# Performance work log

Hardware: AMD Instinct MI355X
Metric: run time of the kernel (lower is better)

The kernel has to match this reference:

```python
import jax, jax.numpy as jnp
import numpy as np

B, T, C = 4, 2048, 1024
H, DK, DV = 16, 64, 64  # num_heads, qk_length, value_length (must be equal per source bug)


def setup_inputs() -> dict:
    key = jax.random.key(0)
    ks = jax.random.split(key, 11)
    s = 0.02
    return {
        "Q": jax.random.normal(ks[0], (B, T, C), jnp.float32),
        "K": jax.random.normal(ks[1], (B, T, C), jnp.float32),
        "V": jax.random.normal(ks[2], (B, T, C), jnp.float32),
        "Wq": jax.random.normal(ks[3], (C, H * DK), jnp.float32) * s,
        "bq": jnp.zeros((H * DK,), jnp.float32),
        "Wk": jax.random.normal(ks[4], (C, H * DK), jnp.float32) * s,
        "bk": jnp.zeros((H * DK,), jnp.float32),
        "Wv": jax.random.normal(ks[5], (C, H * DK), jnp.float32) * s,
        "bv": jnp.zeros((H * DK,), jnp.float32),
        "Wo": jax.random.normal(ks[6], (H * DV, C), jnp.float32) * s,
        "bo": jnp.zeros((C,), jnp.float32),
    }


def _split_heads(x, d):
    # (B, T, H*d) -> (B, H, T, d)
    b, t, _ = x.shape
    return x.reshape(b, t, H, d).transpose(0, 2, 1, 3)


def reference(Q, K, V, Wq, bq, Wk, bk, Wv, bv, Wo, bo):
    q = _split_heads(Q @ Wq + bq, DK)  # (B,H,T,DK)
    k = _split_heads(K @ Wk + bk, DK)
    v = _split_heads(V @ Wv + bv, DV)
    scores = jnp.einsum("bhqd,bhkd->bhqk", q, k) / jnp.sqrt(jnp.float32(DK))
    weights = jax.nn.softmax(scores, axis=-1)  # materialized (B,H,T,T) as in source
    attn = jnp.einsum("bhqk,bhkd->bhqd", weights, v)  # (B,H,T,DV)
    # Faithful to source combine_heads: raw view (B,H,T,DV) -> (B,T,H*DV) WITHOUT transposing
    out = attn.reshape(B, T, H * DV)
    return out @ Wo + bo
```

## Files before the change

kernel.cpp:

```cpp
#include <hip/hip_runtime.h>

typedef unsigned short u16;
typedef __attribute__((ext_vector_type(8))) short bf16x8;
typedef __attribute__((ext_vector_type(4))) float f32x4;

__device__ __forceinline__ u16 f2bf(float f) {
  union { float fv; unsigned u; } v; v.fv = f;
  unsigned r = v.u + 0x7fffu + ((v.u >> 16) & 1u);
  return (u16)(r >> 16);
}

__device__ __forceinline__ unsigned pkbf(float a, float b) {
  union { float f; unsigned u; } ua, ub;
  ua.f = a; ub.f = b;
  return ((ub.u + 0x8000u) & 0xFFFF0000u) | ((ua.u + 0x8000u) >> 16);
}

__device__ __forceinline__ void gload_lds16(const void* g, void* l) {
  __builtin_amdgcn_global_load_lds(
      (const __attribute__((address_space(1))) unsigned*)g,
      (__attribute__((address_space(3))) unsigned*)l, 16, 0, 0);
}

__device__ __forceinline__ int swz128(int o) { return o ^ ((o >> 3) & 0x70); }
__device__ __forceinline__ int swz64(int o) { return o ^ (((o >> 7) & 3) << 4); }

__global__ __launch_bounds__(256) void transpose_cvt4_kernel(
    const float* __restrict__ W0, const float* __restrict__ W1,
    const float* __restrict__ W2, const float* __restrict__ W3,
    u16* __restrict__ T0, u16* __restrict__ T1,
    u16* __restrict__ T2, u16* __restrict__ T3) {
  __shared__ float tile[32][33];
  const int z = blockIdx.z;
  const float* W = z == 0 ? W0 : z == 1 ? W1 : z == 2 ? W2 : W3;
  u16* WT = z == 0 ? T0 : z == 1 ? T1 : z == 2 ? T2 : T3;
  const int bx = blockIdx.x * 32, by = blockIdx.y * 32;
  const int tx = threadIdx.x, ty = threadIdx.y;
  #pragma unroll
  for (int i = 0; i < 32; i += 8)
    tile[ty + i][tx] = W[(size_t)(by + ty + i) * 1024 + bx + tx];
  __syncthreads();
  #pragma unroll
  for (int i = 0; i < 32; i += 8)
    WT[(size_t)(bx + ty + i) * 1024 + by + tx] = f2bf(tile[tx][ty + i]);
}

__global__ __launch_bounds__(256) void proj_gemm_kernel(
    const float* __restrict__ Qf, const float* __restrict__ Kf,
    const float* __restrict__ Vf,
    const u16* __restrict__ WTq, const u16* __restrict__ WTk,
    const u16* __restrict__ WTv,
    const float* __restrict__ bqp, const float* __restrict__ bkp,
    const float* __restrict__ bvp,
    u16* __restrict__ qhd, u16* __restrict__ khd, u16* __restrict__ vtd) {
  __shared__ u16 As[128 * 32];
  __shared__ u16 Bs[128 * 32];
  const int tid = threadIdx.x;
  const int w = tid >> 6, lane = tid & 63;
  const int wr = w >> 1, wc = w & 1;
  const int l16 = lane & 15, lhi = lane >> 4;
  const int lg = (blockIdx.x & 7) * 192 + (blockIdx.x >> 3);
  const int proj = lg >> 9, inner = lg & 511;
  const int m0 = (inner >> 3) * 128, n0 = (inner & 7) * 128;
  const float* A  = proj == 0 ? Qf : proj == 1 ? Kf : Vf;
  const u16*   BT = proj == 0 ? WTq : proj == 1 ? WTk : WTv;
  const float* bias = proj == 0 ? bqp : proj == 1 ? bkp : bvp;

  const int arow = tid >> 2, ac = (tid & 3) * 8;

  f32x4 acc[4][4] = {};
  float4 pre[2][2];

  auto loadA = [&](int kt) {
    #pragma unroll
    for (int i = 0; i < 2; ++i) {
      const float* ap = A + (size_t)(m0 + arow + i * 64) * 1024 + kt * 32 + ac;
      pre[i][0] = *(const float4*)(ap);
      pre[i][1] = *(const float4*)(ap + 4);
    }
  };

  loadA(0);

  for (int kt = 0; kt < 32; ++kt) {
    #pragma unroll
    for (int i = 0; i < 2; ++i) {
      uint4 pk;
      pk.x = pkbf(pre[i][0].x, pre[i][0].y); pk.y = pkbf(pre[i][0].z, pre[i][0].w);
      pk.z = pkbf(pre[i][1].x, pre[i][1].y); pk.w = pkbf(pre[i][1].z, pre[i][1].w);
      const int lb = (arow + i * 64) * 64 + (tid & 3) * 16;
      *(uint4*)((char*)As + swz64(lb)) = pk;
    }
    #pragma unroll
    for (int i = 0; i < 2; ++i) {
      const int ob = w * 2048 + i * 1024;
      const int os = swz64(ob + (lane << 4));
      const int row = os >> 6, kb = os & 63;
      gload_lds16((const char*)BT + (((size_t)(n0 + row)) << 11) + (kt << 6) + kb,
                  (char*)Bs + ob);
    }
    __syncthreads();
    if (kt < 31) loadA(kt + 1);

    bf16x8 a[4], b[4];
    #pragma unroll
    for (int i = 0; i < 4; ++i)
      a[i] = *(const bf16x8*)((const char*)As +
             swz64((wr * 64 + i * 16 + l16) * 64 + lhi * 16));
    #pragma unroll
    for (int j = 0; j < 4; ++j)
      b[j] = *(const bf16x8*)((const char*)Bs +
             swz64((wc * 64 + j * 16 + l16) * 64 + lhi * 16));
    #pragma unroll
    for (int i = 0; i < 4; ++i)
      #pragma unroll
      for (int j = 0; j < 4; ++j)
        acc[i][j] = __builtin_amdgcn_mfma_f32_16x16x32_bf16(a[i], b[j], acc[i][j], 0, 0, 0);
    __syncthreads();
  }

  #pragma unroll
  for (int i = 0; i < 4; ++i) {
    #pragma unroll
    for (int j = 0; j < 4; ++j) {
      const int n = n0 + wc * 64 + j * 16 + l16;
      const float bn = bias[n];
      #pragma unroll
      for (int r = 0; r < 4; ++r) {
        const int m = m0 + wr * 64 + i * 16 + lhi * 4 + r;
        float v = acc[i][j][r] + bn;
        const int bb = m >> 11, t = m & 2047, h = n >> 6, d = n & 63;
        if (proj == 0) {
          v *= 0.18033688f;
          qhd[((((size_t)bb * 16 + h) * 2048 + t) << 6) + d] = f2bf(v);
        } else if (proj == 1) {
          khd[((((size_t)bb * 16 + h) * 2048 + t) << 6) + d] = f2bf(v);
        } else {
          vtd[(((size_t)bb * 16 + h) * 64 + d) * 2048 + t] = f2bf(v);
        }
      }
    }
  }
}

__global__ __launch_bounds__(256) void out_gemm_kernel(
    const u16* __restrict__ A, const u16* __restrict__ BT,
    const float* __restrict__ bias, float* __restrict__ out) {
  __shared__ u16 As[128 * 32];
  __shared__ u16 Bs[128 * 32];
  const int tid = threadIdx.x;
  const int w = tid >> 6, lane = tid & 63;
  const int wr = w >> 1, wc = w & 1;
  const int l16 = lane & 15, lhi = lane >> 4;
  const int lg = (blockIdx.x & 7) * 64 + (blockIdx.x >> 3);
  const int m0 = (lg >> 3) * 128, n0 = (lg & 7) * 128;

  f32x4 acc[4][4] = {};

  for (int kt = 0; kt < 32; ++kt) {
    #pragma unroll
    for (int i = 0; i < 2; ++i) {
      const int ob = w * 2048 + i * 1024;
      const int os = swz64(ob + (lane << 4));
      const int row = os >> 6, kb = os & 63;
      gload_lds16((const char*)A + (((size_t)(m0 + row)) << 11) + (kt << 6) + kb,
                  (char*)As + ob);
      gload_lds16((const char*)BT + (((size_t)(n0 + row)) << 11) + (kt << 6) + kb,
                  (char*)Bs + ob);
    }
    __syncthreads();
    bf16x8 a[4], b[4];
    #pragma unroll
    for (int i = 0; i < 4; ++i)
      a[i] = *(const bf16x8*)((const char*)As +
             swz64((wr * 64 + i * 16 + l16) * 64 + lhi * 16));
    #pragma unroll
    for (int j = 0; j < 4; ++j)
      b[j] = *(const bf16x8*)((const char*)Bs +
             swz64((wc * 64 + j * 16 + l16) * 64 + lhi * 16));
    #pragma unroll
    for (int i = 0; i < 4; ++i)
      #pragma unroll
      for (int j = 0; j < 4; ++j)
        acc[i][j] = __builtin_amdgcn_mfma_f32_16x16x32_bf16(a[i], b[j], acc[i][j], 0, 0, 0);
    __syncthreads();
  }

  #pragma unroll
  for (int i = 0; i < 4; ++i) {
    #pragma unroll
    for (int j = 0; j < 4; ++j) {
      const int n = n0 + wc * 64 + j * 16 + l16;
      const float bn = bias[n];
      #pragma unroll
      for (int r = 0; r < 4; ++r) {
        const int m = m0 + wr * 64 + i * 16 + lhi * 4 + r;
        out[(size_t)m * 1024 + n] = acc[i][j][r] + bn;
      }
    }
  }
}

__global__ __launch_bounds__(512) void attn_kernel(
    const u16* __restrict__ qh, const u16* __restrict__ kh,
    const u16* __restrict__ vth, u16* __restrict__ outPre) {
  __shared__ u16 Kbuf[2][64 * 64];
  __shared__ u16 Vbuf[64 * 64];
  __shared__ u16 Pl[8][16 * 64];

  const int tid = threadIdx.x, w = tid >> 6, lane = tid & 63;
  const int l16 = lane & 15, lhi = lane >> 4;

  const int wg = (blockIdx.x & 7) * 128 + (blockIdx.x >> 3);
  const int qt = wg & 15, hb = wg >> 4;
  const int h = hb & 15, b = hb >> 4;

  const size_t bh = (size_t)b * 16 + h;
  const u16* qb = qh + bh * (2048 * 64);
  const u16* kb = kh + bh * (2048 * 64);
  const u16* vb = vth + bh * (64 * 2048);

  const int qr0 = qt * 128 + w * 16;
  bf16x8 aq[2];
  #pragma unroll
  for (int c = 0; c < 2; ++c)
    aq[c] = *(const bf16x8*)(qb + (qr0 + l16) * 64 + c * 32 + lhi * 8);

  bf16x8 ones;
  #pragma unroll
  for (int e = 0; e < 8; ++e) ones[e] = (short)0x3F80;

  f32x4 acc_o[4] = {};
  f32x4 acc_l = {};

  auto stageK = [&](int buf, int kv) {
    char* Kt = (char*)&Kbuf[buf][0];
    const int ob = w * 1024;
    const int os = swz128(ob + (lane << 4));
    gload_lds16((const char*)kb + ((size_t)kv << 7) + os, Kt + ob);
  };
  auto stageV = [&](int kv) {
    char* Vt = (char*)&Vbuf[0];
    const int ob = w * 1024;
    const int os = swz128(ob + (lane << 4));
    const int dd = os >> 7, j0 = (os & 127) >> 1;
    gload_lds16((const char*)vb + ((size_t)dd << 12) + (((size_t)(kv + j0)) << 1),
                Vt + ob);
  };

  stageK(0, 0);

  for (int t = 0; t < 32; ++t) {
    const int buf = t & 1;
    __syncthreads();
    stageV(t * 64);

    const char* Kt = (const char*)&Kbuf[buf][0];

    f32x4 s[4];
    #pragma unroll
    for (int jt = 0; jt < 4; ++jt) s[jt] = f32x4{-4.f, -4.f, -4.f, -4.f};
    __builtin_amdgcn_s_setprio(1);
    #pragma unroll
    for (int c = 0; c < 2; ++c) {
      #pragma unroll
      for (int jt = 0; jt < 4; ++jt) {
        const bf16x8 bk = *(const bf16x8*)(Kt +
            swz128((jt * 16 + l16) * 128 + c * 64 + lhi * 16));
        s[jt] = __builtin_amdgcn_mfma_f32_16x16x32_bf16(aq[c], bk, s[jt], 0, 0, 0);
      }
    }
    __builtin_amdgcn_s_setprio(0);

    #pragma unroll
    for (int jt = 0; jt < 4; ++jt)
      #pragma unroll
      for (int r = 0; r < 4; ++r)
        s[jt][r] = __builtin_amdgcn_exp2f(s[jt][r]);

    char* Pw = (char*)&Pl[w][0];
    #pragma unroll
    for (int jt = 0; jt < 4; ++jt)
      #pragma unroll
      for (int r = 0; r < 4; ++r) {
        union { float f; unsigned u; } pv;
        pv.f = s[jt][r];
        *(u16*)(Pw + swz128((lhi * 4 + r) * 128 + (jt * 16 + l16) * 2)) =
            (u16)((pv.u + 0x8000u) >> 16);
      }

    __syncthreads();
    if (t < 31) stageK(buf ^ 1, (t + 1) * 64);

    const char* Vt = (const char*)&Vbuf[0];

    __builtin_amdgcn_s_setprio(1);
    #pragma unroll
    for (int c = 0; c < 2; ++c) {
      const bf16x8 ap = *(const bf16x8*)(Pw +
          swz128(l16 * 128 + c * 64 + lhi * 16));
      acc_l = __builtin_amdgcn_mfma_f32_16x16x32_bf16(ap, ones, acc_l, 0, 0, 0);
      #pragma unroll
      for (int dt = 0; dt < 4; ++dt) {
        const bf16x8 bv = *(const bf16x8*)(Vt +
            swz128((dt * 16 + l16) * 128 + c * 64 + lhi * 16));
        acc_o[dt] = __builtin_amdgcn_mfma_f32_16x16x32_bf16(ap, bv, acc_o[dt], 0, 0, 0);
      }
    }
    __builtin_amdgcn_s_setprio(0);
  }

  #pragma unroll
  for (int dt = 0; dt < 4; ++dt) {
    #pragma unroll
    for (int r = 0; r < 4; ++r) {
      const int t = qr0 + lhi * 4 + r;
      const int d = dt * 16 + l16;
      const float v = acc_o[dt][r] / acc_l[r];
      const int rr = h * 128 + (t >> 4);
      const int cc = ((t & 15) << 6) + d;
      outPre[((size_t)b * 2048 + rr) * 1024 + cc] = f2bf(v);
    }
  }
}

extern "C" void kernel_launch(void* const* d_in, const int* in_sizes, int n_in,
                              void* d_out, int out_size, void* d_ws, size_t ws_size,
                              hipStream_t stream) {
  const float* Q  = (const float*)d_in[0];
  const float* K  = (const float*)d_in[1];
  const float* V  = (const float*)d_in[2];
  const float* Wq = (const float*)d_in[3];
  const float* bq = (const float*)d_in[4];
  const float* Wk = (const float*)d_in[5];
  const float* bk = (const float*)d_in[6];
  const float* Wv = (const float*)d_in[7];
  const float* bv = (const float*)d_in[8];
  const float* Wo = (const float*)d_in[9];
  const float* bo = (const float*)d_in[10];

  char* ws = (char*)d_ws;
  const size_t ACT = 16777216;
  u16* act = (u16*)(ws);
  u16* qhd = (u16*)(ws + ACT);
  u16* khd = (u16*)(ws + 2 * ACT);
  u16* vtd = (u16*)(ws + 3 * ACT);
  u16* wtq = (u16*)(ws);
  u16* wtk = (u16*)(ws + 2097152);
  u16* wtv = (u16*)(ws + 2 * 2097152);
  u16* wto = (u16*)(ws + 4 * ACT);

  transpose_cvt4_kernel<<<dim3(32, 32, 4), dim3(32, 8), 0, stream>>>(
      Wq, Wk, Wv, Wo, wtq, wtk, wtv, wto);
  proj_gemm_kernel<<<1536, 256, 0, stream>>>(Q, K, V, wtq, wtk, wtv,
                                             bq, bk, bv, qhd, khd, vtd);
  attn_kernel<<<1024, 512, 0, stream>>>(qhd, khd, vtd, act);
  out_gemm_kernel<<<512, 256, 0, stream>>>(act, wto, bo, (float*)d_out);
}
```

Measured before the change: 241.5 us.

## Double-buffer projection GEMM with K=64 tiles; attention warps handle 32 query rows

The projection GEMM now uses K-tiles of 64 with double-buffered LDS for A and B. The next tile's B loads and A prefetch are issued before the current tile's MFMAs, leaving one barrier per iteration instead of two. The attention kernel drops to 256 threads, with each wave processing two 16-row query blocks, so every K/V fragment read from LDS feeds twice as many MFMAs. The cost is higher register use and more LDS per block, which may lower occupancy.

```diff
diff --git a/kernel.cpp b/kernel.cpp
--- a/kernel.cpp
+++ b/kernel.cpp
@@ -53,8 +53,8 @@
     const float* __restrict__ bqp, const float* __restrict__ bkp,
     const float* __restrict__ bvp,
     u16* __restrict__ qhd, u16* __restrict__ khd, u16* __restrict__ vtd) {
-  __shared__ u16 As[128 * 32];
-  __shared__ u16 Bs[128 * 32];
+  __shared__ u16 As[2][128 * 64];
+  __shared__ u16 Bs[2][128 * 64];
   const int tid = threadIdx.x;
   const int w = tid >> 6, lane = tid & 63;
   const int wr = w >> 1, wc = w & 1;
@@ -66,57 +66,68 @@
   const u16*   BT = proj == 0 ? WTq : proj == 1 ? WTk : WTv;
   const float* bias = proj == 0 ? bqp : proj == 1 ? bkp : bvp;
 
-  const int arow = tid >> 2, ac = (tid & 3) * 8;
+  const int ar = tid >> 3;
+  const int acb = (tid & 7) * 16;
+  const int ael = (tid & 7) * 8;
 
   f32x4 acc[4][4] = {};
-  float4 pre[2][2];
+  float4 pre[4][2];
 
   auto loadA = [&](int kt) {
     #pragma unroll
-    for (int i = 0; i < 2; ++i) {
-      const float* ap = A + (size_t)(m0 + arow + i * 64) * 1024 + kt * 32 + ac;
+    for (int i = 0; i < 4; ++i) {
+      const float* ap = A + (size_t)(m0 + ar + i * 32) * 1024 + kt * 64 + ael;
       pre[i][0] = *(const float4*)(ap);
       pre[i][1] = *(const float4*)(ap + 4);
     }
   };
-
-  loadA(0);
-
-  for (int kt = 0; kt < 32; ++kt) {
-    #pragma unroll
-    for (int i = 0; i < 2; ++i) {
+  auto packA = [&](int bb) {
+    #pragma unroll
+    for (int i = 0; i < 4; ++i) {
       uint4 pk;
       pk.x = pkbf(pre[i][0].x, pre[i][0].y); pk.y = pkbf(pre[i][0].z, pre[i][0].w);
       pk.z = pkbf(pre[i][1].x, pre[i][1].y); pk.w = pkbf(pre[i][1].z, pre[i][1].w);
-      const int lb = (arow + i * 64) * 64 + (tid & 3) * 16;
-      *(uint4*)((char*)As + swz64(lb)) = pk;
-    }
-    #pragma unroll
-    for (int i = 0; i < 2; ++i) {
-      const int ob = w * 2048 + i * 1024;
-      const int os = swz64(ob + (lane << 4));
-      const int row = os >> 6, kb = os & 63;
-      gload_lds16((const char*)BT + (((size_t)(n0 + row)) << 11) + (kt << 6) + kb,
-                  (char*)Bs + ob);
-    }
-    __syncthreads();
-    if (kt < 31) loadA(kt + 1);
-
-    bf16x8 a[4], b[4];
-    #pragma unroll
-    for (int i = 0; i < 4; ++i)
-      a[i] = *(const bf16x8*)((const char*)As +
-             swz64((wr * 64 + i * 16 + l16) * 64 + lhi * 16));
-    #pragma unroll
-    for (int j = 0; j < 4; ++j)
-      b[j] = *(const bf16x8*)((const char*)Bs +
-             swz64((wc * 64 + j * 16 + l16) * 64 + lhi * 16));
-    #pragma unroll
-    for (int i = 0; i < 4; ++i)
+      *(uint4*)((char*)&As[bb][0] + swz128((ar + i * 32) * 128 + acb)) = pk;
+    }
+  };
+  auto stageB = [&](int bb, int kt) {
+    #pragma unroll
+    for (int i = 0; i < 4; ++i) {
+      const int ob = w * 4096 + i * 1024;
+      const int os = swz128(ob + (lane << 4));
+      const int row = os >> 7, cb = os & 127;
+      gload_lds16((const char*)BT + (((size_t)(n0 + row)) << 11) + (kt << 7) + cb,
+                  (char*)&Bs[bb][0] + ob);
+    }
+  };
+
+  loadA(0);
+  stageB(0, 0);
+  packA(0);
+
+  for (int kt = 0; kt < 16; ++kt) {
+    const int bb = kt & 1;
+    __syncthreads();
+    if (kt < 15) { stageB(bb ^ 1, kt + 1); loadA(kt + 1); }
+
+    #pragma unroll
+    for (int s = 0; s < 2; ++s) {
+      bf16x8 a[4], b[4];
+      #pragma unroll
+      for (int i = 0; i < 4; ++i)
+        a[i] = *(const bf16x8*)((const char*)&As[bb][0] +
+               swz128((wr * 64 + i * 16 + l16) * 128 + s * 64 + lhi * 16));
       #pragma unroll
       for (int j = 0; j < 4; ++j)
-        acc[i][j] = __builtin_amdgcn_mfma_f32_16x16x32_bf16(a[i], b[j], acc[i][j], 0, 0, 0);
-    __syncthreads();
+        b[j] = *(const bf16x8*)((const char*)&Bs[bb][0] +
+               swz128((wc * 64 + j * 16 + l16) * 128 + s * 64 + lhi * 16));
+      #pragma unroll
+      for (int i = 0; i < 4; ++i)
+        #pragma unroll
+        for (int j = 0; j < 4; ++j)
+          acc[i][j] = __builtin_amdgcn_mfma_f32_16x16x32_bf16(a[i], b[j], acc[i][j], 0, 0, 0);
+    }
+    if (kt < 15) packA(bb ^ 1);
   }
 
   #pragma unroll
@@ -129,14 +140,14 @@
       for (int r = 0; r < 4; ++r) {
         const int m = m0 + wr * 64 + i * 16 + lhi * 4 + r;
         float v = acc[i][j][r] + bn;
-        const int bb = m >> 11, t = m & 2047, h = n >> 6, d = n & 63;
+        const int bb2 = m >> 11, t = m & 2047, h = n >> 6, d = n & 63;
         if (proj == 0) {
           v *= 0.18033688f;
-          qhd[((((size_t)bb * 16 + h) * 2048 + t) << 6) + d] = f2bf(v);
+          qhd[((((size_t)bb2 * 16 + h) * 2048 + t) << 6) + d] = f2bf(v);
         } else if (proj == 1) {
-          khd[((((size_t)bb * 16 + h) * 2048 + t) << 6) + d] = f2bf(v);
+          khd[((((size_t)bb2 * 16 + h) * 2048 + t) << 6) + d] = f2bf(v);
         } else {
-          vtd[(((size_t)bb * 16 + h) * 64 + d) * 2048 + t] = f2bf(v);
+          vtd[(((size_t)bb2 * 16 + h) * 64 + d) * 2048 + t] = f2bf(v);
         }
       }
     }
@@ -201,12 +212,12 @@
   }
 }
 
-__global__ __launch_bounds__(512) void attn_kernel(
+__global__ __launch_bounds__(256) void attn_kernel(
     const u16* __restrict__ qh, const u16* __restrict__ kh,
     const u16* __restrict__ vth, u16* __restrict__ outPre) {
   __shared__ u16 Kbuf[2][64 * 64];
   __shared__ u16 Vbuf[64 * 64];
-  __shared__ u16 Pl[8][16 * 64];
+  __shared__ u16 Pl[4][32 * 64];
 
   const int tid = threadIdx.x, w = tid >> 6, lane = tid & 63;
   const int l16 = lane & 15, lhi = lane >> 4;
@@ -220,32 +231,40 @@
   const u16* kb = kh + bh * (2048 * 64);
   const u16* vb = vth + bh * (64 * 2048);
 
-  const int qr0 = qt * 128 + w * 16;
-  bf16x8 aq[2];
-  #pragma unroll
-  for (int c = 0; c < 2; ++c)
-    aq[c] = *(const bf16x8*)(qb + (qr0 + l16) * 64 + c * 32 + lhi * 8);
+  const int qr0 = qt * 128 + w * 32;
+  bf16x8 aq[2][2];
+  #pragma unroll
+  for (int u = 0; u < 2; ++u)
+    #pragma unroll
+    for (int c = 0; c < 2; ++c)
+      aq[u][c] = *(const bf16x8*)(qb + (qr0 + u * 16 + l16) * 64 + c * 32 + lhi * 8);
 
   bf16x8 ones;
   #pragma unroll
   for (int e = 0; e < 8; ++e) ones[e] = (short)0x3F80;
 
-  f32x4 acc_o[4] = {};
-  f32x4 acc_l = {};
+  f32x4 acc_o[2][4] = {};
+  f32x4 acc_l[2] = {};
 
   auto stageK = [&](int buf, int kv) {
     char* Kt = (char*)&Kbuf[buf][0];
-    const int ob = w * 1024;
-    const int os = swz128(ob + (lane << 4));
-    gload_lds16((const char*)kb + ((size_t)kv << 7) + os, Kt + ob);
+    #pragma unroll
+    for (int i = 0; i < 2; ++i) {
+      const int ob = w * 2048 + i * 1024;
+      const int os = swz128(ob + (lane << 4));
+      gload_lds16((const char*)kb + ((size_t)kv << 7) + os, Kt + ob);
+    }
   };
   auto stageV = [&](int kv) {
     char* Vt = (char*)&Vbuf[0];
-    const int ob = w * 1024;
-    const int os = swz128(ob + (lane << 4));
-    const int dd = os >> 7, j0 = (os & 127) >> 1;
-    gload_lds16((const char*)vb + ((size_t)dd << 12) + (((size_t)(kv + j0)) << 1),
-                Vt + ob);
+    #pragma unroll
+    for (int i = 0; i < 2; ++i) {
+      const int ob = w * 2048 + i * 1024;
+      const int os = swz128(ob + (lane << 4));
+      const int dd = os >> 7, j0 = (os & 127) >> 1;
+      gload_lds16((const char*)vb + ((size_t)dd << 12) + (((size_t)(kv + j0)) << 1),
+                  Vt + ob);
+    }
   };
 
   stageK(0, 0);
@@ -257,9 +276,11 @@
 
     const char* Kt = (const char*)&Kbuf[buf][0];
 
-    f32x4 s[4];
-    #pragma unroll
-    for (int jt = 0; jt < 4; ++jt) s[jt] = f32x4{-4.f, -4.f, -4.f, -4.f};
+    f32x4 s[2][4];
+    #pragma unroll
+    for (int u = 0; u < 2; ++u)
+      #pragma unroll
+      for (int jt = 0; jt < 4; ++jt) s[u][jt] = f32x4{-4.f, -4.f, -4.f, -4.f};
     __builtin_amdgcn_s_setprio(1);
     #pragma unroll
     for (int c = 0; c < 2; ++c) {
@@ -267,27 +288,32 @@
       for (int jt = 0; jt < 4; ++jt) {
         const bf16x8 bk = *(const bf16x8*)(Kt +
             swz128((jt * 16 + l16) * 128 + c * 64 + lhi * 16));
-        s[jt] = __builtin_amdgcn_mfma_f32_16x16x32_bf16(aq[c], bk, s[jt], 0, 0, 0);
+        s[0][jt] = __builtin_amdgcn_mfma_f32_16x16x32_bf16(aq[0][c], bk, s[0][jt], 0, 0, 0);
+        s[1][jt] = __builtin_amdgcn_mfma_f32_16x16x32_bf16(aq[1][c], bk, s[1][jt], 0, 0, 0);
       }
     }
     __builtin_amdgcn_s_setprio(0);
 
     #pragma unroll
-    for (int jt = 0; jt < 4; ++jt)
-      #pragma unroll
-      for (int r = 0; r < 4; ++r)
-        s[jt][r] = __builtin_amdgcn_exp2f(s[jt][r]);
+    for (int u = 0; u < 2; ++u)
+      #pragma unroll
+      for (int jt = 0; jt < 4; ++jt)
+        #pragma unroll
+        for (int r = 0; r < 4; ++r)
+          s[u][jt][r] = __builtin_amdgcn_exp2f(s[u][jt][r]);
 
     char* Pw = (char*)&Pl[w][0];
     #pragma unroll
-    for (int jt = 0; jt < 4; ++jt)
-      #pragma unroll
-      for (int r = 0; r < 4; ++r) {
-        union { float f; unsigned u; } pv;
-        pv.f = s[jt][r];
-        *(u16*)(Pw + swz128((lhi * 4 + r) * 128 + (jt * 16 + l16) * 2)) =
-            (u16)((pv.u + 0x8000u) >> 16);
-      }
+    for (int u = 0; u < 2; ++u)
+      #pragma unroll
+      for (int jt = 0; jt < 4; ++jt)
+        #pragma unroll
+        for (int r = 0; r < 4; ++r) {
+          union { float f; unsigned u32; } pv;
+          pv.f = s[u][jt][r];
+          *(u16*)(Pw + swz128((u * 16 + lhi * 4 + r) * 128 + (jt * 16 + l16) * 2)) =
+              (u16)((pv.u32 + 0x8000u) >> 16);
+        }
 
     __syncthreads();
     if (t < 31) stageK(buf ^ 1, (t + 1) * 64);
@@ -297,31 +323,36 @@
     __builtin_amdgcn_s_setprio(1);
     #pragma unroll
     for (int c = 0; c < 2; ++c) {
-      const bf16x8 ap = *(const bf16x8*)(Pw +
+      const bf16x8 ap0 = *(const bf16x8*)(Pw +
           swz128(l16 * 128 + c * 64 + lhi * 16));
-      acc_l = __builtin_amdgcn_mfma_f32_16x16x32_bf16(ap, ones, acc_l, 0, 0, 0);
+      const bf16x8 ap1 = *(const bf16x8*)(Pw +
+          swz128((16 + l16) * 128 + c * 64 + lhi * 16));
+      acc_l[0] = __builtin_amdgcn_mfma_f32_16x16x32_bf16(ap0, ones, acc_l[0], 0, 0, 0);
+      acc_l[1] = __builtin_amdgcn_mfma_f32_16x16x32_bf16(ap1, ones, acc_l[1], 0, 0, 0);
       #pragma unroll
       for (int dt = 0; dt < 4; ++dt) {
         const bf16x8 bv = *(const bf16x8*)(Vt +
             swz128((dt * 16 + l16) * 128 + c * 64 + lhi * 16));
-        acc_o[dt] = __builtin_amdgcn_mfma_f32_16x16x32_bf16(ap, bv, acc_o[dt], 0, 0, 0);
+        acc_o[0][dt] = __builtin_amdgcn_mfma_f32_16x16x32_bf16(ap0, bv, acc_o[0][dt], 0, 0, 0);
+        acc_o[1][dt] = __builtin_amdgcn_mfma_f32_16x16x32_bf16(ap1, bv, acc_o[1][dt], 0, 0, 0);
       }
     }
     __builtin_amdgcn_s_setprio(0);
   }
 
   #pragma unroll
-  for (int dt = 0; dt < 4; ++dt) {
-    #pragma unroll
-    for (int r = 0; r < 4; ++r) {
-      const int t = qr0 + lhi * 4 + r;
-      const int d = dt * 16 + l16;
-      const float v = acc_o[dt][r] / acc_l[r];
-      const int rr = h * 128 + (t >> 4);
-      const int cc = ((t & 15) << 6) + d;
-      outPre[((size_t)b * 2048 + rr) * 1024 + cc] = f2bf(v);
-    }
-  }
+  for (int u = 0; u < 2; ++u)
+    #pragma unroll
+    for (int dt = 0; dt < 4; ++dt)
+      #pragma unroll
+      for (int r = 0; r < 4; ++r) {
+        const int t = qr0 + u * 16 + lhi * 4 + r;
+        const int d = dt * 16 + l16;
+        const float v = acc_o[u][dt][r] / acc_l[u][r];
+        const int rr = h * 128 + (t >> 4);
+        const int cc = ((t & 15) << 6) + d;
+        outPre[((size_t)b * 2048 + rr) * 1024 + cc] = f2bf(v);
+      }
 }
 
 extern "C" void kernel_launch(void* const* d_in, const int* in_sizes, int n_in,
@@ -354,6 +385,6 @@
       Wq, Wk, Wv, Wo, wtq, wtk, wtv, wto);
   proj_gemm_kernel<<<1536, 256, 0, stream>>>(Q, K, V, wtq, wtk, wtv,
                                              bq, bk, bv, qhd, khd, vtd);
-  attn_kernel<<<1024, 512, 0, stream>>>(qhd, khd, vtd, act);
+  attn_kernel<<<1024, 256, 0, stream>>>(qhd, khd, vtd, act);
   out_gemm_kernel<<<512, 256, 0, stream>>>(act, wto, bo, (float*)d_out);
 }
```

After: 268.5 us. +11.2%, slower.
